# Optimization experiments

Measured on AMD Instinct MI355X. Metric: run time of the kernel, lower is better.

Reference implementation:

```python
import jax, jax.numpy as jnp
import numpy as np

NUM_HEADS = 8
DIM = 64
DEPTH = DIM // NUM_HEADS  # 8
F = 64  # input feature dim


def setup_inputs() -> dict:
    key = jax.random.key(0)
    ks = jax.random.split(key, 5)
    x = jax.random.normal(ks[0], (4, 2048, F), dtype=jnp.float32)
    # per-head weights stacked: [H, F, depth]; initializer 'normal' ~ N(0, 0.05) in keras,
    # but scale does not change the math structure; use small normal.
    Wq = jax.random.normal(ks[1], (NUM_HEADS, F, DEPTH), dtype=jnp.float32) * 0.05
    Wk = jax.random.normal(ks[2], (NUM_HEADS, F, DEPTH), dtype=jnp.float32) * 0.05
    Wv = jax.random.normal(ks[3], (NUM_HEADS, F, DEPTH), dtype=jnp.float32) * 0.05
    Wo = jax.random.normal(ks[4], (NUM_HEADS * DEPTH, F), dtype=jnp.float32) * 0.05
    return {"x": x, "Wq": Wq, "Wk": Wk, "Wv": Wv, "Wo": Wo}


def reference(x, Wq, Wk, Wv, Wo):
    # x: [B, S, F]; Wq/Wk/Wv: [H, F, D]; Wo: [H*D, F]
    q = jnp.einsum("bsf,hfd->hbsd", x, Wq)
    k = jnp.einsum("bsf,hfd->hbsd", x, Wk)
    v = jnp.einsum("bsf,hfd->hbsd", x, Wv)
    scores = jnp.einsum("hbsd,hbtd->hbst", q, k) / jnp.sqrt(jnp.float32(DEPTH))
    weights = jax.nn.softmax(scores, axis=-1)  # [H, B, S, S]
    heads = jnp.einsum("hbst,hbtd->hbsd", weights, v)  # [H, B, S, D]
    # concat heads along last dim -> [B, S, H*D]
    B, S = x.shape[0], x.shape[1]
    concat = jnp.transpose(heads, (1, 2, 0, 3)).reshape(B, S, NUM_HEADS * DEPTH)
    out = concat @ Wo  # [B, S, F]
    # return_sequences=False -> sum over sequence axis
    return jnp.sum(out, axis=1), weights
```

## Files before the change

### kernel.cpp

```cpp
#include <hip/hip_runtime.h>
#include <cstdint>
#include <cstddef>

#define NH 8
#define NB 4
#define SS 2048
#define FF 64
#define DD 8
#define QKV_SZ (NH*NB*SS*DD)

__device__ __forceinline__ float wave_sum64(float x) {
#define DPP_STEP(ctrl, rm) { int t_ = __builtin_amdgcn_update_dpp(0, __float_as_int(x), (ctrl), (rm), 0xf, true); x += __int_as_float(t_); }
  DPP_STEP(0x111, 0xf)
  DPP_STEP(0x112, 0xf)
  DPP_STEP(0x114, 0xf)
  DPP_STEP(0x118, 0xf)
  DPP_STEP(0x142, 0xa)
  DPP_STEP(0x143, 0xc)
#undef DPP_STEP
  return x;
}

__global__ __launch_bounds__(256) void qkv_kernel(
    const float* __restrict__ x,
    const float* __restrict__ Wq, const float* __restrict__ Wk, const float* __restrict__ Wv,
    float* __restrict__ Qo, float* __restrict__ Ko, float* __restrict__ Vo) {
  __shared__ float xT[64][65];
  const int tid = threadIdx.x;
  const int row0 = blockIdx.x * 64;
  #pragma unroll
  for (int k = 0; k < 4; ++k) {
    int flat4 = tid + 256 * k;
    int r = flat4 >> 4, fq = flat4 & 15;
    float4 xv = reinterpret_cast<const float4*>(x)[(size_t)(row0 + r) * 16 + fq];
    xT[fq * 4 + 0][r] = xv.x; xT[fq * 4 + 1][r] = xv.y;
    xT[fq * 4 + 2][r] = xv.z; xT[fq * 4 + 3][r] = xv.w;
  }
  __syncthreads();
  const int r = tid & 63;
  const int g = __builtin_amdgcn_readfirstlane(tid >> 6);
  const int obase = g * 24 + blockIdx.y * 96;
  float acc[24];
  #pragma unroll
  for (int i = 0; i < 24; ++i) acc[i] = 0.f;
  for (int f = 0; f < 64; ++f) {
    float xv = xT[f][r];
    #pragma unroll
    for (int i = 0; i < 24; ++i) {
      int o = obase + i;
      const float* Wsel = (o < 64) ? Wq : ((o < 128) ? Wk : Wv);
      int oc = o & 63;
      acc[i] = fmaf(xv, Wsel[((oc >> 3) << 9) + f * 8 + (oc & 7)], acc[i]);
    }
  }
  const int row = row0 + r;
  const int b = row >> 11, s = row & 2047;
  const float qscale = 0.35355339059327373f;
  #pragma unroll
  for (int i = 0; i < 24; ++i) {
    int o = obase + i;
    int m = o >> 6, oc = o & 63, h = oc >> 3, d = oc & 7;
    float v = acc[i];
    if (m == 0) v *= qscale;
    float* dst = (m == 0) ? Qo : ((m == 1) ? Ko : Vo);
    dst[(((size_t)(h * NB + b) * SS) + s) * DD + d] = v;
  }
}

__global__ __launch_bounds__(256, 4) void attn_kernel(
    const float* __restrict__ Qg, const float* __restrict__ Kg, const float* __restrict__ Vg,
    float* __restrict__ wOut, float* __restrict__ hsum2) {
  __shared__ float4 klds[4 * 512];
  __shared__ float4 qlds[128];
  __shared__ float psum[4][64];
  __shared__ float rinv_s[64];
  __shared__ float hred[4][8];
  const int tid = threadIdx.x;
  const int lane = tid & 63;
  const int w = tid >> 6;
  const int bx = blockIdx.x;
  const int hb = bx >> 5;
  const int rt = bx & 31;
  const int r0 = rt * 64;
  const float* Kbase = Kg + (size_t)hb * SS * DD;
  const float* Vbase = Vg + (size_t)hb * SS * DD;
  const float4* K4 = reinterpret_cast<const float4*>(Kbase);
  const float4* Q4 = reinterpret_cast<const float4*>(Qg + (size_t)hb * SS * DD + (size_t)r0 * DD);
  float* wBase = wOut + (size_t)hb * SS * SS + (size_t)r0 * SS;

  if (tid < 128) qlds[tid] = Q4[tid];

  float4 qa = Q4[lane * 2], qb = Q4[lane * 2 + 1];
  const float q0 = qa.x, q1 = qa.y, q2 = qa.z, q3 = qa.w;
  const float q4_ = qb.x, q5 = qb.y, q6 = qb.z, q7 = qb.w;
  float rs0 = 0.f, rs1 = 0.f;
  float4* kw = klds + w * 512;
  for (int cc = 0; cc < 2; ++cc) {
    const int t0 = (w * 2 + cc) * 256;
    #pragma unroll
    for (int i = 0; i < 8; ++i) kw[lane + 64 * i] = K4[(size_t)t0 * 2 + lane + 64 * i];
    float4 a0 = kw[0], b0 = kw[1], a1 = kw[2], b1 = kw[3];
    #pragma unroll 2
    for (int tt = 0; tt < 256; tt += 2) {
      const int tn = (tt + 2 < 256) ? (tt + 2) : 254;
      float4 na0 = kw[2 * tn], nb0 = kw[2 * tn + 1];
      float4 na1 = kw[2 * tn + 2], nb1 = kw[2 * tn + 3];
      float s0 = q0 * a0.x;
      s0 = fmaf(q1, a0.y, s0); s0 = fmaf(q2, a0.z, s0); s0 = fmaf(q3, a0.w, s0);
      s0 = fmaf(q4_, b0.x, s0); s0 = fmaf(q5, b0.y, s0); s0 = fmaf(q6, b0.z, s0);
      s0 = fmaf(q7, b0.w, s0);
      float s1 = q0 * a1.x;
      s1 = fmaf(q1, a1.y, s1); s1 = fmaf(q2, a1.z, s1); s1 = fmaf(q3, a1.w, s1);
      s1 = fmaf(q4_, b1.x, s1); s1 = fmaf(q5, b1.y, s1); s1 = fmaf(q6, b1.z, s1);
      s1 = fmaf(q7, b1.w, s1);
      rs0 += __expf(s0);
      rs1 += __expf(s1);
      a0 = na0; b0 = nb0; a1 = na1; b1 = nb1;
    }
  }
  psum[w][lane] = rs0 + rs1;
  __syncthreads();
  if (tid < 64)
    rinv_s[tid] = 1.0f / (psum[0][tid] + psum[1][tid] + psum[2][tid] + psum[3][tid]);
  __syncthreads();

  float A[8] = {0.f, 0.f, 0.f, 0.f, 0.f, 0.f, 0.f, 0.f};
  for (int ci = 0; ci < 4; ++ci) {
    const int c = w * 4 + ci;
    const int tbase = c * 128;
    const float4* kp = reinterpret_cast<const float4*>(Kbase + (size_t)(tbase + 2 * lane) * DD);
    float4 k0a = kp[0], k0b = kp[1], k1a = kp[2], k1b = kp[3];
    float4 qa2 = qlds[0], qb2 = qlds[1];
    float cs0 = 0.f, cs1 = 0.f;
    for (int r = 0; r < 64; ++r) {
      const int rn = (r < 63) ? (r + 1) : 63;
      float4 na = qlds[rn * 2], nb = qlds[rn * 2 + 1];
      const float rin = rinv_s[r];
      float s0 = qa2.x * k0a.x;
      s0 = fmaf(qa2.y, k0a.y, s0); s0 = fmaf(qa2.z, k0a.z, s0); s0 = fmaf(qa2.w, k0a.w, s0);
      s0 = fmaf(qb2.x, k0b.x, s0); s0 = fmaf(qb2.y, k0b.y, s0); s0 = fmaf(qb2.z, k0b.z, s0);
      s0 = fmaf(qb2.w, k0b.w, s0);
      float s1 = qa2.x * k1a.x;
      s1 = fmaf(qa2.y, k1a.y, s1); s1 = fmaf(qa2.z, k1a.z, s1); s1 = fmaf(qa2.w, k1a.w, s1);
      s1 = fmaf(qb2.x, k1b.x, s1); s1 = fmaf(qb2.y, k1b.y, s1); s1 = fmaf(qb2.z, k1b.z, s1);
      s1 = fmaf(qb2.w, k1b.w, s1);
      float p0 = __expf(s0) * rin;
      float p1 = __expf(s1) * rin;
      reinterpret_cast<float2*>(wBase + (size_t)r * SS + tbase)[lane] = make_float2(p0, p1);
      cs0 += p0; cs1 += p1;
      qa2 = na; qb2 = nb;
    }
    const float4* vp = reinterpret_cast<const float4*>(Vbase + (size_t)(tbase + 2 * lane) * DD);
    float4 v0a = vp[0], v0b = vp[1], v1a = vp[2], v1b = vp[3];
    A[0] = fmaf(cs0, v0a.x, A[0]); A[0] = fmaf(cs1, v1a.x, A[0]);
    A[1] = fmaf(cs0, v0a.y, A[1]); A[1] = fmaf(cs1, v1a.y, A[1]);
    A[2] = fmaf(cs0, v0a.z, A[2]); A[2] = fmaf(cs1, v1a.z, A[2]);
    A[3] = fmaf(cs0, v0a.w, A[3]); A[3] = fmaf(cs1, v1a.w, A[3]);
    A[4] = fmaf(cs0, v0b.x, A[4]); A[4] = fmaf(cs1, v1b.x, A[4]);
    A[5] = fmaf(cs0, v0b.y, A[5]); A[5] = fmaf(cs1, v1b.y, A[5]);
    A[6] = fmaf(cs0, v0b.z, A[6]); A[6] = fmaf(cs1, v1b.z, A[6]);
    A[7] = fmaf(cs0, v0b.w, A[7]); A[7] = fmaf(cs1, v1b.w, A[7]);
  }

  #pragma unroll
  for (int d = 0; d < 8; ++d) {
    float t = wave_sum64(A[d]);
    if (lane == 63) hred[w][d] = t;
  }
  __syncthreads();
  if (tid < 8) {
    float t = hred[0][tid] + hred[1][tid] + hred[2][tid] + hred[3][tid];
    hsum2[(size_t)bx * 8 + tid] = t;
  }
}

__global__ __launch_bounds__(256) void out_kernel(
    const float* __restrict__ hsum2, const float* __restrict__ Wo,
    float* __restrict__ out) {
  __shared__ float ch[256];
  const int tid = threadIdx.x;
  {
    int hb = tid >> 3, d = tid & 7;
    float s = 0.f;
    for (int rtile = 0; rtile < 32; ++rtile) s += hsum2[(size_t)(hb * 32 + rtile) * 8 + d];
    ch[tid] = s;
  }
  __syncthreads();
  const int b = tid >> 6, f = tid & 63;
  float acc = 0.f;
  for (int h = 0; h < 8; ++h) {
    #pragma unroll
    for (int d = 0; d < 8; ++d) {
      acc = fmaf(ch[(h * 4 + b) * 8 + d], Wo[(h * 8 + d) * 64 + f], acc);
    }
  }
  out[b * 64 + f] = acc;
}

extern "C" void kernel_launch(void* const* d_in, const int* in_sizes, int n_in,
                              void* d_out, int out_size, void* d_ws, size_t ws_size,
                              hipStream_t stream) {
  const float* x  = (const float*)d_in[0];
  const float* Wq = (const float*)d_in[1];
  const float* Wk = (const float*)d_in[2];
  const float* Wv = (const float*)d_in[3];
  const float* Wo = (const float*)d_in[4];
  float* out = (float*)d_out;
  float* wts = out + 256;
  float* ws = (float*)d_ws;
  float* Q = ws;
  float* K = ws + QKV_SZ;
  float* V = ws + 2 * (size_t)QKV_SZ;
  float* hs = ws + 3 * (size_t)QKV_SZ;

  qkv_kernel<<<dim3(128, 2), 256, 0, stream>>>(x, Wq, Wk, Wv, Q, K, V);
  attn_kernel<<<1024, 256, 0, stream>>>(Q, K, V, wts, hs);
  out_kernel<<<1, 256, 0, stream>>>(hs, Wo, out);
}
```

Measured before the change: 613.8 us.

## Vectorize QKV weight loads, widen attention tiles, fold softmax normalization into exponent

The QKV projection now gives each wave three whole (matrix, head) column groups. It loads weights as float4 and writes Q/K/V with float4 stores instead of scalar accesses. The attention kernel processes four keys per lane in both passes, so probability rows are written as float4 instead of float2. The reciprocal multiply is replaced by subtracting log(rowsum) inside the exponent, which removes one multiply per element and slightly changes rounding. Register pressure rises from holding more K/V values per lane.

Measured after the change: 582.5 us. 1.05x faster.

```diff
diff --git a/kernel.cpp b/kernel.cpp
--- a/kernel.cpp
+++ b/kernel.cpp
@@ -38,32 +38,45 @@
   }
   __syncthreads();
   const int r = tid & 63;
-  const int g = __builtin_amdgcn_readfirstlane(tid >> 6);
-  const int obase = g * 24 + blockIdx.y * 96;
-  float acc[24];
-  #pragma unroll
-  for (int i = 0; i < 24; ++i) acc[i] = 0.f;
+  const int wg = __builtin_amdgcn_readfirstlane((int)(blockIdx.y * 4 + (tid >> 6)));
+  const float* Wmh[3];
+  #pragma unroll
+  for (int j = 0; j < 3; ++j) {
+    int c = wg * 3 + j;
+    int m = c >> 3, h = c & 7;
+    const float* Wsel = (m == 0) ? Wq : ((m == 1) ? Wk : Wv);
+    Wmh[j] = Wsel + (h << 9);
+  }
+  float acc[3][8];
+  #pragma unroll
+  for (int j = 0; j < 3; ++j)
+    #pragma unroll
+    for (int d = 0; d < 8; ++d) acc[j][d] = 0.f;
   for (int f = 0; f < 64; ++f) {
     float xv = xT[f][r];
     #pragma unroll
-    for (int i = 0; i < 24; ++i) {
-      int o = obase + i;
-      const float* Wsel = (o < 64) ? Wq : ((o < 128) ? Wk : Wv);
-      int oc = o & 63;
-      acc[i] = fmaf(xv, Wsel[((oc >> 3) << 9) + f * 8 + (oc & 7)], acc[i]);
+    for (int j = 0; j < 3; ++j) {
+      const float4* wp = reinterpret_cast<const float4*>(Wmh[j] + f * 8);
+      float4 wa = wp[0], wb = wp[1];
+      acc[j][0] = fmaf(xv, wa.x, acc[j][0]); acc[j][1] = fmaf(xv, wa.y, acc[j][1]);
+      acc[j][2] = fmaf(xv, wa.z, acc[j][2]); acc[j][3] = fmaf(xv, wa.w, acc[j][3]);
+      acc[j][4] = fmaf(xv, wb.x, acc[j][4]); acc[j][5] = fmaf(xv, wb.y, acc[j][5]);
+      acc[j][6] = fmaf(xv, wb.z, acc[j][6]); acc[j][7] = fmaf(xv, wb.w, acc[j][7]);
     }
   }
   const int row = row0 + r;
   const int b = row >> 11, s = row & 2047;
   const float qscale = 0.35355339059327373f;
   #pragma unroll
-  for (int i = 0; i < 24; ++i) {
-    int o = obase + i;
-    int m = o >> 6, oc = o & 63, h = oc >> 3, d = oc & 7;
-    float v = acc[i];
-    if (m == 0) v *= qscale;
-    float* dst = (m == 0) ? Qo : ((m == 1) ? Ko : Vo);
-    dst[(((size_t)(h * NB + b) * SS) + s) * DD + d] = v;
+  for (int j = 0; j < 3; ++j) {
+    int c = wg * 3 + j;
+    int m = c >> 3, h = c & 7;
+    float sc = (m == 0) ? qscale : 1.f;
+    float* dst = ((m == 0) ? Qo : ((m == 1) ? Ko : Vo)) + (((size_t)(h * NB + b) * SS) + s) * DD;
+    float4 o0 = make_float4(acc[j][0] * sc, acc[j][1] * sc, acc[j][2] * sc, acc[j][3] * sc);
+    float4 o1 = make_float4(acc[j][4] * sc, acc[j][5] * sc, acc[j][6] * sc, acc[j][7] * sc);
+    reinterpret_cast<float4*>(dst)[0] = o0;
+    reinterpret_cast<float4*>(dst)[1] = o1;
   }
 }
 
@@ -73,7 +86,7 @@
   __shared__ float4 klds[4 * 512];
   __shared__ float4 qlds[128];
   __shared__ float psum[4][64];
-  __shared__ float rinv_s[64];
+  __shared__ float nls_s[64];
   __shared__ float hred[4][8];
   const int tid = threadIdx.x;
   const int lane = tid & 63;
@@ -100,11 +113,13 @@
     #pragma unroll
     for (int i = 0; i < 8; ++i) kw[lane + 64 * i] = K4[(size_t)t0 * 2 + lane + 64 * i];
     float4 a0 = kw[0], b0 = kw[1], a1 = kw[2], b1 = kw[3];
-    #pragma unroll 2
-    for (int tt = 0; tt < 256; tt += 2) {
-      const int tn = (tt + 2 < 256) ? (tt + 2) : 254;
-      float4 na0 = kw[2 * tn], nb0 = kw[2 * tn + 1];
+    float4 a2 = kw[4], b2 = kw[5], a3 = kw[6], b3 = kw[7];
+    for (int tt = 0; tt < 256; tt += 4) {
+      const int tn = (tt + 4 < 256) ? (tt + 4) : 0;
+      float4 na0 = kw[2 * tn],     nb0 = kw[2 * tn + 1];
       float4 na1 = kw[2 * tn + 2], nb1 = kw[2 * tn + 3];
+      float4 na2 = kw[2 * tn + 4], nb2 = kw[2 * tn + 5];
+      float4 na3 = kw[2 * tn + 6], nb3 = kw[2 * tn + 7];
       float s0 = q0 * a0.x;
       s0 = fmaf(q1, a0.y, s0); s0 = fmaf(q2, a0.z, s0); s0 = fmaf(q3, a0.w, s0);
       s0 = fmaf(q4_, b0.x, s0); s0 = fmaf(q5, b0.y, s0); s0 = fmaf(q6, b0.z, s0);
@@ -113,53 +128,80 @@
       s1 = fmaf(q1, a1.y, s1); s1 = fmaf(q2, a1.z, s1); s1 = fmaf(q3, a1.w, s1);
       s1 = fmaf(q4_, b1.x, s1); s1 = fmaf(q5, b1.y, s1); s1 = fmaf(q6, b1.z, s1);
       s1 = fmaf(q7, b1.w, s1);
-      rs0 += __expf(s0);
-      rs1 += __expf(s1);
+      float s2 = q0 * a2.x;
+      s2 = fmaf(q1, a2.y, s2); s2 = fmaf(q2, a2.z, s2); s2 = fmaf(q3, a2.w, s2);
+      s2 = fmaf(q4_, b2.x, s2); s2 = fmaf(q5, b2.y, s2); s2 = fmaf(q6, b2.z, s2);
+      s2 = fmaf(q7, b2.w, s2);
+      float s3 = q0 * a3.x;
+      s3 = fmaf(q1, a3.y, s3); s3 = fmaf(q2, a3.z, s3); s3 = fmaf(q3, a3.w, s3);
+      s3 = fmaf(q4_, b3.x, s3); s3 = fmaf(q5, b3.y, s3); s3 = fmaf(q6, b3.z, s3);
+      s3 = fmaf(q7, b3.w, s3);
+      rs0 += __expf(s0) + __expf(s1);
+      rs1 += __expf(s2) + __expf(s3);
       a0 = na0; b0 = nb0; a1 = na1; b1 = nb1;
+      a2 = na2; b2 = nb2; a3 = na3; b3 = nb3;
     }
   }
   psum[w][lane] = rs0 + rs1;
   __syncthreads();
   if (tid < 64)
-    rinv_s[tid] = 1.0f / (psum[0][tid] + psum[1][tid] + psum[2][tid] + psum[3][tid]);
+    nls_s[tid] = -__logf(psum[0][tid] + psum[1][tid] + psum[2][tid] + psum[3][tid]);
   __syncthreads();
 
   float A[8] = {0.f, 0.f, 0.f, 0.f, 0.f, 0.f, 0.f, 0.f};
-  for (int ci = 0; ci < 4; ++ci) {
-    const int c = w * 4 + ci;
-    const int tbase = c * 128;
-    const float4* kp = reinterpret_cast<const float4*>(Kbase + (size_t)(tbase + 2 * lane) * DD);
+  for (int ci = 0; ci < 2; ++ci) {
+    const int c = w * 2 + ci;
+    const int tbase = c * 256;
+    const int tl = tbase + 4 * lane;
+    const float4* kp = reinterpret_cast<const float4*>(Kbase + (size_t)tl * DD);
     float4 k0a = kp[0], k0b = kp[1], k1a = kp[2], k1b = kp[3];
+    float4 k2a = kp[4], k2b = kp[5], k3a = kp[6], k3b = kp[7];
     float4 qa2 = qlds[0], qb2 = qlds[1];
-    float cs0 = 0.f, cs1 = 0.f;
+    float cs0 = 0.f, cs1 = 0.f, cs2 = 0.f, cs3 = 0.f;
     for (int r = 0; r < 64; ++r) {
       const int rn = (r < 63) ? (r + 1) : 63;
       float4 na = qlds[rn * 2], nb = qlds[rn * 2 + 1];
-      const float rin = rinv_s[r];
-      float s0 = qa2.x * k0a.x;
+      const float nl = nls_s[r];
+      float s0 = fmaf(qa2.x, k0a.x, nl);
       s0 = fmaf(qa2.y, k0a.y, s0); s0 = fmaf(qa2.z, k0a.z, s0); s0 = fmaf(qa2.w, k0a.w, s0);
       s0 = fmaf(qb2.x, k0b.x, s0); s0 = fmaf(qb2.y, k0b.y, s0); s0 = fmaf(qb2.z, k0b.z, s0);
       s0 = fmaf(qb2.w, k0b.w, s0);
-      float s1 = qa2.x * k1a.x;
+      float s1 = fmaf(qa2.x, k1a.x, nl);
       s1 = fmaf(qa2.y, k1a.y, s1); s1 = fmaf(qa2.z, k1a.z, s1); s1 = fmaf(qa2.w, k1a.w, s1);
       s1 = fmaf(qb2.x, k1b.x, s1); s1 = fmaf(qb2.y, k1b.y, s1); s1 = fmaf(qb2.z, k1b.z, s1);
       s1 = fmaf(qb2.w, k1b.w, s1);
-      float p0 = __expf(s0) * rin;
-      float p1 = __expf(s1) * rin;
-      reinterpret_cast<float2*>(wBase + (size_t)r * SS + tbase)[lane] = make_float2(p0, p1);
-      cs0 += p0; cs1 += p1;
+      float s2 = fmaf(qa2.x, k2a.x, nl);
+      s2 = fmaf(qa2.y, k2a.y, s2); s2 = fmaf(qa2.z, k2a.z, s2); s2 = fmaf(qa2.w, k2a.w, s2);
+      s2 = fmaf(qb2.x, k2b.x, s2); s2 = fmaf(qb2.y, k2b.y, s2); s2 = fmaf(qb2.z, k2b.z, s2);
+      s2 = fmaf(qb2.w, k2b.w, s2);
+      float s3 = fmaf(qa2.x, k3a.x, nl);
+      s3 = fmaf(qa2.y, k3a.y, s3); s3 = fmaf(qa2.z, k3a.z, s3); s3 = fmaf(qa2.w, k3a.w, s3);
+      s3 = fmaf(qb2.x, k3b.x, s3); s3 = fmaf(qb2.y, k3b.y, s3); s3 = fmaf(qb2.z, k3b.z, s3);
+      s3 = fmaf(qb2.w, k3b.w, s3);
+      float p0 = __expf(s0), p1 = __expf(s1), p2 = __expf(s2), p3 = __expf(s3);
+      reinterpret_cast<float4*>(wBase + (size_t)r * SS + tl)[0] = make_float4(p0, p1, p2, p3);
+      cs0 += p0; cs1 += p1; cs2 += p2; cs3 += p3;
       qa2 = na; qb2 = nb;
     }
-    const float4* vp = reinterpret_cast<const float4*>(Vbase + (size_t)(tbase + 2 * lane) * DD);
+    const float4* vp = reinterpret_cast<const float4*>(Vbase + (size_t)tl * DD);
     float4 v0a = vp[0], v0b = vp[1], v1a = vp[2], v1b = vp[3];
+    float4 v2a = vp[4], v2b = vp[5], v3a = vp[6], v3b = vp[7];
     A[0] = fmaf(cs0, v0a.x, A[0]); A[0] = fmaf(cs1, v1a.x, A[0]);
+    A[0] = fmaf(cs2, v2a.x, A[0]); A[0] = fmaf(cs3, v3a.x, A[0]);
     A[1] = fmaf(cs0, v0a.y, A[1]); A[1] = fmaf(cs1, v1a.y, A[1]);
+    A[1] = fmaf(cs2, v2a.y, A[1]); A[1] = fmaf(cs3, v3a.y, A[1]);
     A[2] = fmaf(cs0, v0a.z, A[2]); A[2] = fmaf(cs1, v1a.z, A[2]);
+    A[2] = fmaf(cs2, v2a.z, A[2]); A[2] = fmaf(cs3, v3a.z, A[2]);
     A[3] = fmaf(cs0, v0a.w, A[3]); A[3] = fmaf(cs1, v1a.w, A[3]);
+    A[3] = fmaf(cs2, v2a.w, A[3]); A[3] = fmaf(cs3, v3a.w, A[3]);
     A[4] = fmaf(cs0, v0b.x, A[4]); A[4] = fmaf(cs1, v1b.x, A[4]);
+    A[4] = fmaf(cs2, v2b.x, A[4]); A[4] = fmaf(cs3, v3b.x, A[4]);
     A[5] = fmaf(cs0, v0b.y, A[5]); A[5] = fmaf(cs1, v1b.y, A[5]);
+    A[5] = fmaf(cs2, v2b.y, A[5]); A[5] = fmaf(cs3, v3b.y, A[5]);
     A[6] = fmaf(cs0, v0b.z, A[6]); A[6] = fmaf(cs1, v1b.z, A[6]);
+    A[6] = fmaf(cs2, v2b.z, A[6]); A[6] = fmaf(cs3, v3b.z, A[6]);
     A[7] = fmaf(cs0, v0b.w, A[7]); A[7] = fmaf(cs1, v1b.w, A[7]);
+    A[7] = fmaf(cs2, v2b.w, A[7]); A[7] = fmaf(cs3, v3b.w, A[7]);
   }
 
   #pragma unroll
```
